# Kernel tuning notes

Measured on AMD Instinct MI355X. Metric: run time of the kernel, lower is better.

Reference implementation:

```python
import jax, jax.numpy as jnp
import numpy as np

NEG_BIG = -9e15  # matches torch's -9000000000000000.0 mask value


def setup_inputs() -> dict:
    key = jax.random.key(0)
    k0, k1, k2, k3 = jax.random.split(key, 4)
    B, N, F_IN, F_OUT = 8, 2048, 128, 128
    h = jax.random.normal(k0, (B, N, F_IN), dtype=jnp.float32)
    adj = jax.random.randint(k1, (B, N, N), 0, 2, dtype=jnp.int32)
    W = jax.random.normal(k2, (F_IN, F_OUT), dtype=jnp.float32) * 0.05
    a = jax.random.normal(k3, (2 * F_OUT,), dtype=jnp.float32) * 0.05
    return {"h": h, "adj": adj, "W": W, "a": a}


def reference(h, adj, W, a):
    # Wh: [B, N, F_out]
    Wh = jnp.einsum("bnf,fo->bno", h, W)
    f_out = Wh.shape[-1]
    # a @ [Wh_i || Wh_j] == (a1 @ Wh_i) + (a2 @ Wh_j): avoids O(N^2 * 2F) concat
    a1, a2 = a[:f_out], a[f_out:]
    src = jnp.einsum("bno,o->bn", Wh, a1)  # row (i) contribution
    dst = jnp.einsum("bno,o->bn", Wh, a2)  # col (j) contribution
    e = jax.nn.leaky_relu(src[:, :, None] + dst[:, None, :], negative_slope=0.2)
    e = jnp.where(adj > 0, e, NEG_BIG)
    attention = jax.nn.softmax(e, axis=-1)  # dropout is identity at eval time
    h_prime = jnp.einsum("bij,bjo->bio", attention, Wh)
    return h_prime
```

## Files before the change

kernel.cpp:

```cpp
#include <hip/hip_runtime.h>
#include <hip/hip_bf16.h>

#define BB 8
#define NN 2048
#define FF 128

typedef __bf16 bf16x8 __attribute__((ext_vector_type(8)));
typedef float f32x4 __attribute__((ext_vector_type(4)));
typedef float f32x16 __attribute__((ext_vector_type(16)));

__device__ __forceinline__ void gload_lds16(const void* g, void* l) {
    __builtin_amdgcn_global_load_lds(
        (const __attribute__((address_space(1))) unsigned int*)g,
        (__attribute__((address_space(3))) unsigned int*)l, 16, 0, 0);
}

__global__ __launch_bounds__(256) void wh_kernel(
    const float* __restrict__ h, const float* __restrict__ W,
    const float* __restrict__ a, __bf16* __restrict__ fragB,
    float* __restrict__ srcg, float* __restrict__ dstg)
{
    __shared__ float  s_h[32][132];
    __shared__ __bf16 s_wh[32][132];
    __shared__ float  s_s[2][32];
    __shared__ float  s_d[2][32];

    const int bid = blockIdx.x;
    const int b   = bid >> 6;
    const int J   = bid & 63;
    const int r0  = J * 32;
    const int t   = threadIdx.x;
    const int w   = t >> 6;
    const int l   = t & 63;
    const int itile = w & 1;
    const int fh    = w >> 1;
    const int g     = l >> 4;
    const int c16   = l & 15;

#pragma unroll
    for (int i = 0; i < 4; ++i) {
        const int idx = t + i * 256;
        const int r   = idx >> 5;
        const int c4  = idx & 31;
        *(f32x4*)&s_h[r][c4 * 4] =
            *(const f32x4*)(h + (size_t)(b * NN + r0 + r) * FF + c4 * 4);
    }
    __syncthreads();

    const float* hrow = &s_h[itile * 16 + c16][0];
    f32x4 acc[4] = {};

#pragma unroll
    for (int kt = 0; kt < 4; ++kt) {
        const int k0 = kt * 32 + g * 8;
        f32x4 h0 = *(const f32x4*)(hrow + k0);
        f32x4 h1 = *(const f32x4*)(hrow + k0 + 4);
        bf16x8 af;
        af[0]=(__bf16)h0[0]; af[1]=(__bf16)h0[1]; af[2]=(__bf16)h0[2]; af[3]=(__bf16)h0[3];
        af[4]=(__bf16)h1[0]; af[5]=(__bf16)h1[1]; af[6]=(__bf16)h1[2]; af[7]=(__bf16)h1[3];
#pragma unroll
        for (int ft = 0; ft < 4; ++ft) {
            const int c = (fh * 4 + ft) * 16 + c16;
            bf16x8 bf;
#pragma unroll
            for (int e = 0; e < 8; ++e) bf[e] = (__bf16)W[(k0 + e) * FF + c];
            acc[ft] = __builtin_amdgcn_mfma_f32_16x16x32_bf16(af, bf, acc[ft], 0, 0, 0);
        }
    }

    float a1v[4], a2v[4];
#pragma unroll
    for (int ft = 0; ft < 4; ++ft) {
        const int c = (fh * 4 + ft) * 16 + c16;
        a1v[ft] = a[c];
        a2v[ft] = a[FF + c];
    }
#pragma unroll
    for (int r = 0; r < 4; ++r) {
        float s = 0.f, d2 = 0.f;
#pragma unroll
        for (int ft = 0; ft < 4; ++ft) {
            s  += acc[ft][r] * a1v[ft];
            d2 += acc[ft][r] * a2v[ft];
        }
#pragma unroll
        for (int m = 1; m <= 8; m <<= 1) {
            s  += __shfl_xor(s,  m);
            d2 += __shfl_xor(d2, m);
        }
        if (c16 == 0) {
            s_s[fh][itile * 16 + g * 4 + r] = s;
            s_d[fh][itile * 16 + g * 4 + r] = d2;
        }
    }

#pragma unroll
    for (int ft = 0; ft < 4; ++ft)
#pragma unroll
        for (int r = 0; r < 4; ++r)
            s_wh[itile * 16 + g * 4 + r][(fh * 4 + ft) * 16 + c16] = (__bf16)acc[ft][r];

    __syncthreads();

#pragma unroll
    for (int e2 = 0; e2 < 2; ++e2) {
        const int ent  = t + e2 * 256;
        const int tile = ent >> 6;
        const int jl   = tile >> 2;
        const int ft   = tile & 3;
        const int lE   = ent & 63;
        const int rowE = jl * 16 + (lE >> 5) * 8;
        const int colE = ft * 32 + (lE & 31);
        bf16x8 v;
#pragma unroll
        for (int ee = 0; ee < 8; ++ee) v[ee] = s_wh[rowE + ee][colE];
        *(bf16x8*)(fragB + (((size_t)(b * 128 + J * 2 + jl) * 4 + ft) * 64 + lE) * 8) = v;
    }

    if (t < 32) {
        srcg[b * NN + r0 + t] = s_s[0][t] + s_s[1][t];
        dstg[b * NN + r0 + t] = s_d[0][t] + s_d[1][t];
    }
}

__global__ __launch_bounds__(256, 2) void attn_kernel(
    const int* __restrict__ adj, const __bf16* __restrict__ fragB,
    const float* __restrict__ srcg, const float* __restrict__ dstg,
    float* __restrict__ out)
{
    __shared__ char s_all[74240];

    const int bid0 = blockIdx.x;
    const int bid  = (bid0 & 7) * 64 + (bid0 >> 3);
    const int b    = bid >> 6;
    const int I0   = (bid & 63) * 32;
    const int t    = threadIdx.x;
    const int q    = t >> 6;
    const int l    = t & 63;
    const int r31  = l & 31;
    const int hi   = l >> 5;

    char* awave = s_all + q * 8192;
    char* fwave = s_all + 32768 + q * 8192;
    char* dstw  = s_all + 65536 + q * 2048;
    float* s_ps = (float*)(s_all + 73728);

    const float sv = srcg[b * NN + I0 + r31];
    asm volatile("s_waitcnt vmcnt(0) lgkmcnt(0)" ::: "memory");

    const char* aSrc = (const char*)adj
        + ((size_t)(b * NN + I0 + r31) * NN + q * 512) * 4 + hi * 32;
    const char* fBase = (const char*)fragB
        + (size_t)(b * 128 + q * 32) * 4096 + (size_t)l * 16;
    const char* dSrc = (const char*)(dstg + (size_t)b * NN + q * 512) + l * 16;

#define ISSUE_A(ki_, sl_) {                                                   \
        const char* pa_ = aSrc + (size_t)(ki_) * 64;                          \
        gload_lds16(pa_,      awave + (sl_) * 2048 + l * 16);                 \
        gload_lds16(pa_ + 16, awave + (sl_) * 2048 + 1024 + l * 16); }
#define ISSUE_F(ki_, sl_) {                                                   \
        const char* pf_ = fBase + (size_t)(ki_) * 4096;                       \
        char* fd_ = fwave + (sl_) * 4096 + l * 16;                            \
        gload_lds16(pf_,        fd_);                                         \
        gload_lds16(pf_ + 1024, fd_ + 1024);                                  \
        gload_lds16(pf_ + 2048, fd_ + 2048);                                  \
        gload_lds16(pf_ + 3072, fd_ + 3072); }

    gload_lds16(dSrc,        dstw + l * 16);
    gload_lds16(dSrc + 1024, dstw + 1024 + l * 16);
    ISSUE_A(0, 0);
    ISSUE_F(0, 0);
    ISSUE_A(1, 1);

    f32x16 acc0 = {}, acc1 = {}, acc2 = {}, acc3 = {};
    float psum = 0.f;

#pragma unroll 4
    for (int kt = 0; kt < 32; ++kt) {
        const int kF = (kt + 1 < 32) ? kt + 1 : 31;
        const int kA = (kt + 2 < 32) ? kt + 2 : 31;
        ISSUE_F(kF, (kt + 1) & 1);
        ISSUE_A(kA, (kt + 2) & 3);
        asm volatile("s_waitcnt vmcnt(8)" ::: "memory");
        __builtin_amdgcn_sched_barrier(0);

        const char* asl = awave + (kt & 3) * 2048 + l * 16;
        const int4 A0 = *(const int4*)(asl);
        const int4 A1 = *(const int4*)(asl + 1024);
        const f32x4 d0 = *(const f32x4*)(dstw + kt * 64 + hi * 32);
        const f32x4 d1 = *(const f32x4*)(dstw + kt * 64 + hi * 32 + 16);
        const int   am[8] = {A0.x, A0.y, A0.z, A0.w, A1.x, A1.y, A1.z, A1.w};
        const float dv[8] = {d0[0], d0[1], d0[2], d0[3], d1[0], d1[1], d1[2], d1[3]};

        bf16x8 af;
#pragma unroll
        for (int e = 0; e < 8; ++e) {
            float x = sv + dv[e];
            x = fmaxf(x, 0.2f * x);
            float p = __expf(x);
            p = (am[e] > 0) ? p : 0.f;
            psum += p;
            af[e] = (__bf16)p;
        }

        const char* fsl = fwave + (kt & 1) * 4096 + l * 16;
        const bf16x8 b0 = *(const bf16x8*)(fsl);
        const bf16x8 b1 = *(const bf16x8*)(fsl + 1024);
        const bf16x8 b2 = *(const bf16x8*)(fsl + 2048);
        const bf16x8 b3 = *(const bf16x8*)(fsl + 3072);
        acc0 = __builtin_amdgcn_mfma_f32_32x32x16_bf16(af, b0, acc0, 0, 0, 0);
        acc1 = __builtin_amdgcn_mfma_f32_32x32x16_bf16(af, b1, acc1, 0, 0, 0);
        acc2 = __builtin_amdgcn_mfma_f32_32x32x16_bf16(af, b2, acc2, 0, 0, 0);
        acc3 = __builtin_amdgcn_mfma_f32_32x32x16_bf16(af, b3, acc3, 0, 0, 0);
    }
#undef ISSUE_A
#undef ISSUE_F

    asm volatile("s_waitcnt vmcnt(0)" ::: "memory");

    psum += __shfl_xor(psum, 32);
    if (l < 32) s_ps[q * 32 + l] = psum;

    __syncthreads();
    float* comb = (float*)s_all;
    {
        float* cb = comb + ((q * 4 + 0) * 64 + l) * 17;
#pragma unroll
        for (int r = 0; r < 16; ++r) cb[r] = acc0[r];
        cb = comb + ((q * 4 + 1) * 64 + l) * 17;
#pragma unroll
        for (int r = 0; r < 16; ++r) cb[r] = acc1[r];
        cb = comb + ((q * 4 + 2) * 64 + l) * 17;
#pragma unroll
        for (int r = 0; r < 16; ++r) cb[r] = acc2[r];
        cb = comb + ((q * 4 + 3) * 64 + l) * 17;
#pragma unroll
        for (int r = 0; r < 16; ++r) cb[r] = acc3[r];
    }
    __syncthreads();

    f32x16 tot;
#pragma unroll
    for (int r = 0; r < 16; ++r)
        tot[r] = comb[((0 * 4 + q) * 64 + l) * 17 + r]
               + comb[((1 * 4 + q) * 64 + l) * 17 + r]
               + comb[((2 * 4 + q) * 64 + l) * 17 + r]
               + comb[((3 * 4 + q) * 64 + l) * 17 + r];

    const float dtot = s_ps[0 * 32 + r31] + s_ps[1 * 32 + r31]
                     + s_ps[2 * 32 + r31] + s_ps[3 * 32 + r31];
    const float rin  = 1.f / dtot;

#pragma unroll
    for (int r = 0; r < 16; ++r) {
        const int row  = (r & 3) + 8 * (r >> 2) + 4 * hi;
        const float dv2 = __shfl(rin, row);
        out[(size_t)(b * NN + I0 + row) * FF + q * 32 + r31] = tot[r] * dv2;
    }
}

extern "C" void kernel_launch(void* const* d_in, const int* in_sizes, int n_in,
                              void* d_out, int out_size, void* d_ws, size_t ws_size,
                              hipStream_t stream)
{
    const float* h   = (const float*)d_in[0];
    const int*   adj = (const int*)d_in[1];
    const float* W   = (const float*)d_in[2];
    const float* a   = (const float*)d_in[3];
    float* out = (float*)d_out;

    char* ws = (char*)d_ws;
    __bf16* fragB = (__bf16*)ws;
    float*  srcg  = (float*)(ws + (4 << 20));
    float*  dstg  = (float*)(ws + (4 << 20) + (64 << 10));

    wh_kernel<<<512, 256, 0, stream>>>(h, W, a, fragB, srcg, dstg);
    attn_kernel<<<512, 256, 0, stream>>>(adj, fragB, srcg, dstg, out);
}
```

Before: 42.32 us.

## Load Wh fragments straight into registers with a 4-deep prefetch, shrink LDS

The bf16 Wh B-operand fragments are now fetched with global_load_dwordx4 directly into VGPRs and rotated through four register sets (3 steps of prefetch), instead of being staged through LDS with a double buffer. This removes the LDS round trip and the LDS reads for the B operand and cuts shared memory from about 74KB to about 41KB. To fit the smaller LDS, the cross-wave reduction of accumulators is done in two halves with extra barriers. The trade-off is higher register pressure from 16 fragment registers, which may hurt occupancy at launch_bounds(256,2), plus a couple more syncs in the epilogue.

```diff
diff --git a/kernel.cpp b/kernel.cpp
--- a/kernel.cpp
+++ b/kernel.cpp
@@ -128,7 +128,7 @@
     const float* __restrict__ srcg, const float* __restrict__ dstg,
     float* __restrict__ out)
 {
-    __shared__ char s_all[74240];
+    __shared__ char s_all[41472];
 
     const int bid0 = blockIdx.x;
     const int bid  = (bid0 & 7) * 64 + (bid0 >> 3);
@@ -141,9 +141,8 @@
     const int hi   = l >> 5;
 
     char* awave = s_all + q * 8192;
-    char* fwave = s_all + 32768 + q * 8192;
-    char* dstw  = s_all + 65536 + q * 2048;
-    float* s_ps = (float*)(s_all + 73728);
+    char* dstw  = s_all + 32768 + q * 2048;
+    float* s_ps = (float*)(s_all + 40960);
 
     const float sv = srcg[b * NN + I0 + r31];
     asm volatile("s_waitcnt vmcnt(0) lgkmcnt(0)" ::: "memory");
@@ -154,98 +153,113 @@
         + (size_t)(b * 128 + q * 32) * 4096 + (size_t)l * 16;
     const char* dSrc = (const char*)(dstg + (size_t)b * NN + q * 512) + l * 16;
 
-#define ISSUE_A(ki_, sl_) {                                                   \
+#define ISSUE_F(ki_, B0_, B1_, B2_, B3_) {                                    \
+        const char* pf_ = fBase + (size_t)(ki_) * 4096;                       \
+        asm volatile("global_load_dwordx4 %0, %1, off"                        \
+                     : "=&v"(B0_) : "v"(pf_));                                \
+        asm volatile("global_load_dwordx4 %0, %1, off offset:1024"            \
+                     : "=&v"(B1_) : "v"(pf_));                                \
+        asm volatile("global_load_dwordx4 %0, %1, off offset:2048"            \
+                     : "=&v"(B2_) : "v"(pf_));                                \
+        asm volatile("global_load_dwordx4 %0, %1, off offset:3072"            \
+                     : "=&v"(B3_) : "v"(pf_)); }
+#define ISSUE_A(ki_) {                                                        \
         const char* pa_ = aSrc + (size_t)(ki_) * 64;                          \
-        gload_lds16(pa_,      awave + (sl_) * 2048 + l * 16);                 \
-        gload_lds16(pa_ + 16, awave + (sl_) * 2048 + 1024 + l * 16); }
-#define ISSUE_F(ki_, sl_) {                                                   \
-        const char* pf_ = fBase + (size_t)(ki_) * 4096;                       \
-        char* fd_ = fwave + (sl_) * 4096 + l * 16;                            \
-        gload_lds16(pf_,        fd_);                                         \
-        gload_lds16(pf_ + 1024, fd_ + 1024);                                  \
-        gload_lds16(pf_ + 2048, fd_ + 2048);                                  \
-        gload_lds16(pf_ + 3072, fd_ + 3072); }
+        gload_lds16(pa_,      awave + ((ki_) & 3) * 2048 + l * 16);           \
+        gload_lds16(pa_ + 16, awave + ((ki_) & 3) * 2048 + 1024 + l * 16); }
+
+    bf16x8 fA0, fA1, fA2, fA3, fB0, fB1, fB2, fB3;
+    bf16x8 fC0, fC1, fC2, fC3, fD0, fD1, fD2, fD3;
+    f32x16 acc0 = {}, acc1 = {}, acc2 = {}, acc3 = {};
+    float psum = 0.f;
 
     gload_lds16(dSrc,        dstw + l * 16);
     gload_lds16(dSrc + 1024, dstw + 1024 + l * 16);
-    ISSUE_A(0, 0);
-    ISSUE_F(0, 0);
-    ISSUE_A(1, 1);
-
-    f32x16 acc0 = {}, acc1 = {}, acc2 = {}, acc3 = {};
-    float psum = 0.f;
-
-#pragma unroll 4
-    for (int kt = 0; kt < 32; ++kt) {
-        const int kF = (kt + 1 < 32) ? kt + 1 : 31;
-        const int kA = (kt + 2 < 32) ? kt + 2 : 31;
-        ISSUE_F(kF, (kt + 1) & 1);
-        ISSUE_A(kA, (kt + 2) & 3);
-        asm volatile("s_waitcnt vmcnt(8)" ::: "memory");
-        __builtin_amdgcn_sched_barrier(0);
-
-        const char* asl = awave + (kt & 3) * 2048 + l * 16;
-        const int4 A0 = *(const int4*)(asl);
-        const int4 A1 = *(const int4*)(asl + 1024);
-        const f32x4 d0 = *(const f32x4*)(dstw + kt * 64 + hi * 32);
-        const f32x4 d1 = *(const f32x4*)(dstw + kt * 64 + hi * 32 + 16);
-        const int   am[8] = {A0.x, A0.y, A0.z, A0.w, A1.x, A1.y, A1.z, A1.w};
-        const float dv[8] = {d0[0], d0[1], d0[2], d0[3], d1[0], d1[1], d1[2], d1[3]};
-
-        bf16x8 af;
-#pragma unroll
-        for (int e = 0; e < 8; ++e) {
-            float x = sv + dv[e];
-            x = fmaxf(x, 0.2f * x);
-            float p = __expf(x);
-            p = (am[e] > 0) ? p : 0.f;
-            psum += p;
-            af[e] = (__bf16)p;
-        }
-
-        const char* fsl = fwave + (kt & 1) * 4096 + l * 16;
-        const bf16x8 b0 = *(const bf16x8*)(fsl);
-        const bf16x8 b1 = *(const bf16x8*)(fsl + 1024);
-        const bf16x8 b2 = *(const bf16x8*)(fsl + 2048);
-        const bf16x8 b3 = *(const bf16x8*)(fsl + 3072);
-        acc0 = __builtin_amdgcn_mfma_f32_32x32x16_bf16(af, b0, acc0, 0, 0, 0);
-        acc1 = __builtin_amdgcn_mfma_f32_32x32x16_bf16(af, b1, acc1, 0, 0, 0);
-        acc2 = __builtin_amdgcn_mfma_f32_32x32x16_bf16(af, b2, acc2, 0, 0, 0);
-        acc3 = __builtin_amdgcn_mfma_f32_32x32x16_bf16(af, b3, acc3, 0, 0, 0);
-    }
+    ISSUE_F(0, fA0, fA1, fA2, fA3);  ISSUE_A(0);
+    ISSUE_F(1, fB0, fB1, fB2, fB3);  ISSUE_A(1);
+    ISSUE_F(2, fC0, fC1, fC2, fC3);  ISSUE_A(2);
+
+#define STEP(kt_, C0_, C1_, C2_, C3_, I0_, I1_, I2_, I3_) {                   \
+        const int kX_ = ((kt_) + 3 < 32) ? (kt_) + 3 : 31;                    \
+        ISSUE_F(kX_, I0_, I1_, I2_, I3_);                                     \
+        ISSUE_A(kX_);                                                         \
+        asm volatile("s_waitcnt vmcnt(18)" ::: "memory");                     \
+        __builtin_amdgcn_sched_barrier(0);                                    \
+        const char* asl_ = awave + ((kt_) & 3) * 2048 + l * 16;               \
+        const int4 A0_ = *(const int4*)(asl_);                                \
+        const int4 A1_ = *(const int4*)(asl_ + 1024);                         \
+        const f32x4 d0_ = *(const f32x4*)(dstw + (kt_) * 64 + hi * 32);       \
+        const f32x4 d1_ = *(const f32x4*)(dstw + (kt_) * 64 + hi * 32 + 16);  \
+        const int   am_[8] = {A0_.x, A0_.y, A0_.z, A0_.w,                     \
+                              A1_.x, A1_.y, A1_.z, A1_.w};                    \
+        const float dv_[8] = {d0_[0], d0_[1], d0_[2], d0_[3],                 \
+                              d1_[0], d1_[1], d1_[2], d1_[3]};                \
+        bf16x8 af_;                                                           \
+        _Pragma("unroll")                                                     \
+        for (int e = 0; e < 8; ++e) {                                         \
+            float x = sv + dv_[e];                                            \
+            x = fmaxf(x, 0.2f * x);                                           \
+            float p = __expf(x);                                              \
+            p = (am_[e] > 0) ? p : 0.f;                                       \
+            psum += p;                                                        \
+            af_[e] = (__bf16)p;                                               \
+        }                                                                     \
+        acc0 = __builtin_amdgcn_mfma_f32_32x32x16_bf16(af_, C0_, acc0, 0, 0, 0); \
+        acc1 = __builtin_amdgcn_mfma_f32_32x32x16_bf16(af_, C1_, acc1, 0, 0, 0); \
+        acc2 = __builtin_amdgcn_mfma_f32_32x32x16_bf16(af_, C2_, acc2, 0, 0, 0); \
+        acc3 = __builtin_amdgcn_mfma_f32_32x32x16_bf16(af_, C3_, acc3, 0, 0, 0); }
+
+    for (int kt4 = 0; kt4 < 32; kt4 += 4) {
+        STEP(kt4 + 0, fA0, fA1, fA2, fA3, fD0, fD1, fD2, fD3);
+        STEP(kt4 + 1, fB0, fB1, fB2, fB3, fA0, fA1, fA2, fA3);
+        STEP(kt4 + 2, fC0, fC1, fC2, fC3, fB0, fB1, fB2, fB3);
+        STEP(kt4 + 3, fD0, fD1, fD2, fD3, fC0, fC1, fC2, fC3);
+    }
+#undef STEP
+#undef ISSUE_F
 #undef ISSUE_A
-#undef ISSUE_F
-
-    asm volatile("s_waitcnt vmcnt(0)" ::: "memory");
+
+    asm volatile("s_waitcnt vmcnt(0) lgkmcnt(0)" ::: "memory");
 
     psum += __shfl_xor(psum, 32);
     if (l < 32) s_ps[q * 32 + l] = psum;
 
-    __syncthreads();
     float* comb = (float*)s_all;
+    f32x16 tot;
+
+    __syncthreads();
     {
-        float* cb = comb + ((q * 4 + 0) * 64 + l) * 17;
-#pragma unroll
-        for (int r = 0; r < 16; ++r) cb[r] = acc0[r];
-        cb = comb + ((q * 4 + 1) * 64 + l) * 17;
-#pragma unroll
-        for (int r = 0; r < 16; ++r) cb[r] = acc1[r];
-        cb = comb + ((q * 4 + 2) * 64 + l) * 17;
-#pragma unroll
-        for (int r = 0; r < 16; ++r) cb[r] = acc2[r];
-        cb = comb + ((q * 4 + 3) * 64 + l) * 17;
-#pragma unroll
-        for (int r = 0; r < 16; ++r) cb[r] = acc3[r];
-    }
-    __syncthreads();
-
-    f32x16 tot;
-#pragma unroll
-    for (int r = 0; r < 16; ++r)
-        tot[r] = comb[((0 * 4 + q) * 64 + l) * 17 + r]
-               + comb[((1 * 4 + q) * 64 + l) * 17 + r]
-               + comb[((2 * 4 + q) * 64 + l) * 17 + r]
-               + comb[((3 * 4 + q) * 64 + l) * 17 + r];
+        float* c0 = comb + ((q * 2 + 0) * 64 + l) * 17;
+        float* c1 = comb + ((q * 2 + 1) * 64 + l) * 17;
+#pragma unroll
+        for (int r = 0; r < 16; ++r) { c0[r] = acc0[r]; c1[r] = acc1[r]; }
+    }
+    __syncthreads();
+    if (q < 2) {
+#pragma unroll
+        for (int r = 0; r < 16; ++r)
+            tot[r] = comb[((0 * 2 + q) * 64 + l) * 17 + r]
+                   + comb[((1 * 2 + q) * 64 + l) * 17 + r]
+                   + comb[((2 * 2 + q) * 64 + l) * 17 + r]
+                   + comb[((3 * 2 + q) * 64 + l) * 17 + r];
+    }
+    __syncthreads();
+    {
+        float* c0 = comb + ((q * 2 + 0) * 64 + l) * 17;
+        float* c1 = comb + ((q * 2 + 1) * 64 + l) * 17;
+#pragma unroll
+        for (int r = 0; r < 16; ++r) { c0[r] = acc2[r]; c1[r] = acc3[r]; }
+    }
+    __syncthreads();
+    if (q >= 2) {
+        const int f2 = q - 2;
+#pragma unroll
+        for (int r = 0; r < 16; ++r)
+            tot[r] = comb[((0 * 2 + f2) * 64 + l) * 17 + r]
+                   + comb[((1 * 2 + f2) * 64 + l) * 17 + r]
+                   + comb[((2 * 2 + f2) * 64 + l) * 17 + r]
+                   + comb[((3 * 2 + f2) * 64 + l) * 17 + r];
+    }
 
     const float dtot = s_ps[0 * 32 + r31] + s_ps[1 * 32 + r31]
                      + s_ps[2 * 32 + r31] + s_ps[3 * 32 + r31];
```

Result: slower. 44.19 us (+4.4%).

## Stage W through transposed LDS and share cooperative adj/fragB tiles across waves

Applied to the files above, without the earlier changes.

In wh_kernel, W is loaded once into shared memory as a transposed bf16 tile, replacing the per-element strided global loads used to build each MFMA B fragment. In attn_kernel, waves no longer stream private K-slices. Two waves load shared fragB chunks and two load XOR-swizzled adjacency tiles plus dst into a block-wide triple-buffered LDS ring, and a barrier runs every iteration. This is meant to cut redundant global traffic and LDS bank conflicts, at the cost of a block barrier per step, a larger LDS footprint that may lower occupancy, and an asymmetric load split between waves.

```diff
diff --git a/kernel.cpp b/kernel.cpp
--- a/kernel.cpp
+++ b/kernel.cpp
@@ -22,6 +22,7 @@
 {
     __shared__ float  s_h[32][132];
     __shared__ __bf16 s_wh[32][132];
+    __shared__ __bf16 s_Wt[128][136];
     __shared__ float  s_s[2][32];
     __shared__ float  s_d[2][32];
 
@@ -45,6 +46,19 @@
         *(f32x4*)&s_h[r][c4 * 4] =
             *(const f32x4*)(h + (size_t)(b * NN + r0 + r) * FF + c4 * 4);
     }
+    {
+        const int wk  = t >> 1;
+        const int wc0 = (t & 1) * 64;
+        const float* wrow = W + wk * FF + wc0;
+#pragma unroll
+        for (int i = 0; i < 16; ++i) {
+            const f32x4 v = *(const f32x4*)(wrow + i * 4);
+            s_Wt[wc0 + i * 4 + 0][wk] = (__bf16)v[0];
+            s_Wt[wc0 + i * 4 + 1][wk] = (__bf16)v[1];
+            s_Wt[wc0 + i * 4 + 2][wk] = (__bf16)v[2];
+            s_Wt[wc0 + i * 4 + 3][wk] = (__bf16)v[3];
+        }
+    }
     __syncthreads();
 
     const float* hrow = &s_h[itile * 16 + c16][0];
@@ -61,9 +75,7 @@
 #pragma unroll
         for (int ft = 0; ft < 4; ++ft) {
             const int c = (fh * 4 + ft) * 16 + c16;
-            bf16x8 bf;
-#pragma unroll
-            for (int e = 0; e < 8; ++e) bf[e] = (__bf16)W[(k0 + e) * FF + c];
+            const bf16x8 bf = *(const bf16x8*)&s_Wt[c][k0];
             acc[ft] = __builtin_amdgcn_mfma_f32_16x16x32_bf16(af, bf, acc[ft], 0, 0, 0);
         }
     }
@@ -128,7 +140,7 @@
     const float* __restrict__ srcg, const float* __restrict__ dstg,
     float* __restrict__ out)
 {
-    __shared__ char s_all[74240];
+    __shared__ char s_all[81920];
 
     const int bid0 = blockIdx.x;
     const int bid  = (bid0 & 7) * 64 + (bid0 >> 3);
@@ -140,55 +152,78 @@
     const int r31  = l & 31;
     const int hi   = l >> 5;
 
-    char* awave = s_all + q * 8192;
-    char* fwave = s_all + 32768 + q * 8192;
-    char* dstw  = s_all + 65536 + q * 2048;
-    float* s_ps = (float*)(s_all + 73728);
+    float* dstf = (float*)(s_all + 73728);
 
     const float sv = srcg[b * NN + I0 + r31];
     asm volatile("s_waitcnt vmcnt(0) lgkmcnt(0)" ::: "memory");
 
-    const char* aSrc = (const char*)adj
-        + ((size_t)(b * NN + I0 + r31) * NN + q * 512) * 4 + hi * 32;
-    const char* fBase = (const char*)fragB
-        + (size_t)(b * 128 + q * 32) * 4096 + (size_t)l * 16;
-    const char* dSrc = (const char*)(dstg + (size_t)b * NN + q * 512) + l * 16;
-
-#define ISSUE_A(ki_, sl_) {                                                   \
-        const char* pa_ = aSrc + (size_t)(ki_) * 64;                          \
-        gload_lds16(pa_,      awave + (sl_) * 2048 + l * 16);                 \
-        gload_lds16(pa_ + 16, awave + (sl_) * 2048 + 1024 + l * 16); }
-#define ISSUE_F(ki_, sl_) {                                                   \
-        const char* pf_ = fBase + (size_t)(ki_) * 4096;                       \
-        char* fd_ = fwave + (sl_) * 4096 + l * 16;                            \
-        gload_lds16(pf_,        fd_);                                         \
-        gload_lds16(pf_ + 1024, fd_ + 1024);                                  \
-        gload_lds16(pf_ + 2048, fd_ + 2048);                                  \
-        gload_lds16(pf_ + 3072, fd_ + 3072); }
-
-    gload_lds16(dSrc,        dstw + l * 16);
-    gload_lds16(dSrc + 1024, dstw + 1024 + l * 16);
-    ISSUE_A(0, 0);
-    ISSUE_F(0, 0);
-    ISSUE_A(1, 1);
+    const char* fragBB = (const char*)fragB + (size_t)b * 524288;
+    const char* fSrc = fragBB + (size_t)(q & 1) * 8192 + (size_t)l * 16;
+    const int   fDstL = (q & 1) * 8192 + l * 16;
+
+    const char* adjBB = (const char*)adj + (size_t)b * NN * (NN * 4);
+    const int   o0   = (q & 1) * 4;
+    const int   rl0  = o0 * 4 + (l >> 4);
+    const char* aS0 = adjBB + (size_t)(I0 + rl0)      * 8192 + (((l & 15) ^ ((rl0)      & 7)) * 16);
+    const char* aS1 = adjBB + (size_t)(I0 + rl0 + 4)  * 8192 + (((l & 15) ^ ((rl0 + 4)  & 7)) * 16);
+    const char* aS2 = adjBB + (size_t)(I0 + rl0 + 8)  * 8192 + (((l & 15) ^ ((rl0 + 8)  & 7)) * 16);
+    const char* aS3 = adjBB + (size_t)(I0 + rl0 + 12) * 8192 + (((l & 15) ^ ((rl0 + 12) & 7)) * 16);
+    const char* dS  = (const char*)(dstg + (size_t)b * NN) + o0 * 1024 + l * 16;
+
+#define ISSUE_F(wc_, sl_) {                                                   \
+        const char* ps_ = fSrc + (size_t)(wc_) * 16384;                       \
+        char* pd_ = s_all + (sl_) * 16384 + fDstL;                            \
+        _Pragma("unroll")                                                     \
+        for (int i = 0; i < 8; ++i)                                           \
+            gload_lds16(ps_ + i * 1024, pd_ + i * 1024);                      \
+    }
+#define ISSUE_A(wc_, sl_) {                                                   \
+        const size_t wo_ = (size_t)(wc_) * 256;                               \
+        char* pd_ = s_all + 49152 + (sl_) * 8192 + o0 * 1024 + l * 16;        \
+        gload_lds16(aS0 + wo_, pd_);                                          \
+        gload_lds16(aS1 + wo_, pd_ + 1024);                                   \
+        gload_lds16(aS2 + wo_, pd_ + 2048);                                   \
+        gload_lds16(aS3 + wo_, pd_ + 3072);                                   \
+    }
 
     f32x16 acc0 = {}, acc1 = {}, acc2 = {}, acc3 = {};
     float psum = 0.f;
 
-#pragma unroll 4
-    for (int kt = 0; kt < 32; ++kt) {
-        const int kF = (kt + 1 < 32) ? kt + 1 : 31;
-        const int kA = (kt + 2 < 32) ? kt + 2 : 31;
-        ISSUE_F(kF, (kt + 1) & 1);
-        ISSUE_A(kA, (kt + 2) & 3);
-        asm volatile("s_waitcnt vmcnt(8)" ::: "memory");
+    if (q < 2) {
+        ISSUE_F(0, 0);
+    } else {
+        char* dd = (char*)dstf + o0 * 1024 + l * 16;
+#pragma unroll
+        for (int i = 0; i < 4; ++i)
+            gload_lds16(dS + i * 1024, dd + i * 1024);
+        ISSUE_A(0, 0);
+    }
+
+    const int c0 = q * 4 + hi * 2;
+    const int x7 = r31 & 7;
+
+    int scur = 0;
+    for (int w = 0; w < 32; ++w) {
+        const int snext = (scur == 2) ? 0 : scur + 1;
+        const int wn = (w + 1 < 32) ? w + 1 : 31;
+        if (q < 2) {
+            ISSUE_F(wn, snext);
+            asm volatile("s_waitcnt vmcnt(8)" ::: "memory");
+        } else {
+            ISSUE_A(wn, snext);
+            asm volatile("s_waitcnt vmcnt(4)" ::: "memory");
+        }
         __builtin_amdgcn_sched_barrier(0);
-
-        const char* asl = awave + (kt & 3) * 2048 + l * 16;
-        const int4 A0 = *(const int4*)(asl);
-        const int4 A1 = *(const int4*)(asl + 1024);
-        const f32x4 d0 = *(const f32x4*)(dstw + kt * 64 + hi * 32);
-        const f32x4 d1 = *(const f32x4*)(dstw + kt * 64 + hi * 32 + 16);
+        __builtin_amdgcn_s_barrier();
+        __builtin_amdgcn_sched_barrier(0);
+
+        const char* asl = s_all + 49152 + scur * 8192
+                        + (r31 >> 2) * 1024 + (r31 & 3) * 256;
+        const int4 A0 = *(const int4*)(asl + ((c0       ^ x7) * 16));
+        const int4 A1 = *(const int4*)(asl + (((c0 + 1) ^ x7) * 16));
+        const float* dw = dstf + w * 64 + q * 16 + hi * 8;
+        const f32x4 d0 = *(const f32x4*)(dw);
+        const f32x4 d1 = *(const f32x4*)(dw + 4);
         const int   am[8] = {A0.x, A0.y, A0.z, A0.w, A1.x, A1.y, A1.z, A1.w};
         const float dv[8] = {d0[0], d0[1], d0[2], d0[3], d1[0], d1[1], d1[2], d1[3]};
 
@@ -203,7 +238,7 @@
             af[e] = (__bf16)p;
         }
 
-        const char* fsl = fwave + (kt & 1) * 4096 + l * 16;
+        const char* fsl = s_all + scur * 16384 + q * 4096 + l * 16;
         const bf16x8 b0 = *(const bf16x8*)(fsl);
         const bf16x8 b1 = *(const bf16x8*)(fsl + 1024);
         const bf16x8 b2 = *(const bf16x8*)(fsl + 2048);
@@ -212,16 +247,20 @@
         acc1 = __builtin_amdgcn_mfma_f32_32x32x16_bf16(af, b1, acc1, 0, 0, 0);
         acc2 = __builtin_amdgcn_mfma_f32_32x32x16_bf16(af, b2, acc2, 0, 0, 0);
         acc3 = __builtin_amdgcn_mfma_f32_32x32x16_bf16(af, b3, acc3, 0, 0, 0);
-    }
+
+        scur = snext;
+    }
+#undef ISSUE_F
 #undef ISSUE_A
-#undef ISSUE_F
-
-    asm volatile("s_waitcnt vmcnt(0)" ::: "memory");
+
+    asm volatile("s_waitcnt vmcnt(0) lgkmcnt(0)" ::: "memory");
 
     psum += __shfl_xor(psum, 32);
+
+    __syncthreads();
+    float* s_ps = (float*)(s_all + 73728);
     if (l < 32) s_ps[q * 32 + l] = psum;
 
-    __syncthreads();
     float* comb = (float*)s_all;
     {
         float* cb = comb + ((q * 4 + 0) * 64 + l) * 17;
```

New measurement: 44.16 us. 4.3% more time.
